# Kernel optimization log

Hardware: AMD Instinct MI355X
Metric: run time of the kernel (lower is better)

## Reference

```python
import jax, jax.numpy as jnp
import numpy as np

# ---- module config (init_kwargs) ----
B, N = 4, 1
IH, IW = 256, 704          # image_size
FH, FW = 32, 88            # feature_size
C = 80                     # out_channels
XB = (-54.0, 54.0, 0.3)
YB = (-54.0, 54.0, 0.3)
ZB = (-10.0, 10.0, 20.0)
DB = (1.0, 60.0, 0.5)
D = int((DB[1] - DB[0]) / DB[2])   # 118 depth bins
NX = (int((XB[1]-XB[0])/XB[2]), int((YB[1]-YB[0])/YB[2]), int((ZB[1]-ZB[0])/ZB[2]))  # (360,360,1)
DX = jnp.array([XB[2], YB[2], ZB[2]], jnp.float32)
BX = jnp.array([XB[0]+XB[2]/2, YB[0]+YB[2]/2, ZB[0]+ZB[2]/2], jnp.float32)


def _frustum():
    # [D, fH, fW, 3] of (pixel_x, pixel_y, depth)
    ds = jnp.broadcast_to(jnp.arange(DB[0], DB[1], DB[2], dtype=jnp.float32)[:, None, None], (D, FH, FW))
    xs = jnp.broadcast_to(jnp.linspace(0.0, IW - 1.0, FW, dtype=jnp.float32)[None, None, :], (D, FH, FW))
    ys = jnp.broadcast_to(jnp.linspace(0.0, IH - 1.0, FH, dtype=jnp.float32)[None, :, None], (D, FH, FW))
    return jnp.stack([xs, ys, ds], axis=-1)


def _get_geometry(rots, trans, intrins, post_rots, post_trans,
                  l2c_rots, l2c_trans, extra_rots, extra_trans):
    frustum = _frustum()                                       # [D,fH,fW,3]
    # undo image augmentation
    pts = frustum[None, None] - post_trans[:, :, None, None, None, :]          # [B,N,D,fH,fW,3]
    pts = jnp.einsum('bnij,bndhwj->bndhwi', jnp.linalg.inv(post_rots), pts)
    # (u*d, v*d, d)
    pts = jnp.concatenate([pts[..., :2] * pts[..., 2:3], pts[..., 2:3]], axis=-1)
    # camera -> ego (sensor2ego) combined with inverse intrinsics
    combine = jnp.einsum('bnij,bnjk->bnik', rots, jnp.linalg.inv(intrins))
    pts = jnp.einsum('bnij,bndhwj->bndhwi', combine, pts) + trans[:, :, None, None, None, :]
    # ego -> lidar via inverse of lidar2camera (passed in as lidar2ego_* in forward)
    pts = pts - l2c_trans[:, None, None, None, None, :]
    pts = jnp.einsum('bij,bndhwj->bndhwi', jnp.linalg.inv(l2c_rots), pts)
    # lidar augmentation
    pts = jnp.einsum('bij,bndhwj->bndhwi', extra_rots, pts) + extra_trans[:, None, None, None, None, :]
    return pts  # [B,N,D,fH,fW,3]


def _bev_pool(geom, x):
    Bb = x.shape[0]
    Cc = x.shape[-1]
    Np = x.size // Cc                                          # B*N*D*fH*fW
    feats = x.reshape(Np, Cc)
    # voxel coords; torch .long() truncates toward zero, astype(int32) matches
    coords = ((geom - (BX - DX / 2.0)) / DX).reshape(Np, 3).astype(jnp.int32)
    batch_ix = jnp.repeat(jnp.arange(Bb, dtype=jnp.int32), Np // Bb)
    kept = ((coords[:, 0] >= 0) & (coords[:, 0] < NX[0]) &
            (coords[:, 1] >= 0) & (coords[:, 1] < NX[1]) &
            (coords[:, 2] >= 0) & (coords[:, 2] < NX[2]))
    # zero out dropped points instead of filtering (jit-friendly, same sum)
    feats = jnp.where(kept[:, None], feats, 0.0)
    cx = jnp.clip(coords[:, 0], 0, NX[0] - 1)
    cy = jnp.clip(coords[:, 1], 0, NX[1] - 1)
    cz = jnp.clip(coords[:, 2], 0, NX[2] - 1)
    lin = ((batch_ix * NX[2] + cz) * NX[0] + cx) * NX[1] + cy
    grid = jax.ops.segment_sum(feats, lin, num_segments=Bb * NX[2] * NX[0] * NX[1])
    grid = grid.reshape(Bb, NX[2], NX[0], NX[1], Cc)           # (B, Z, X, Y, C)
    # torch: permute(0,4,1,3,2)->(B,C,Z,Y,X), unbind Z, cat on channel => z-major (B, Z*C, Y, X)
    grid = jnp.transpose(grid, (0, 1, 4, 3, 2))                # (B, Z, C, Y, X)
    return grid.reshape(Bb, NX[2] * Cc, NX[1], NX[0])


def setup_inputs() -> dict:
    key = jax.random.key(0)
    k1, k2, k3 = jax.random.split(key, 3)
    x = jax.random.normal(k1, (B, N, D, FH, FW, C), dtype=jnp.float32)
    # sensor2ego: identity (forward's fallback branch)
    rots = jnp.broadcast_to(jnp.eye(3, dtype=jnp.float32), (B, N, 3, 3))
    trans = jnp.zeros((B, N, 3), jnp.float32)
    intr = np.array([[500.0, 0.0, 352.0], [0.0, 500.0, 128.0], [0.0, 0.0, 1.0]], np.float32)
    intrins = jnp.broadcast_to(jnp.asarray(intr), (B, N, 3, 3))
    post_rots = jnp.broadcast_to(jnp.eye(3, dtype=jnp.float32), (B, N, 3, 3))
    post_trans = jax.random.uniform(k2, (B, N, 3), jnp.float32, -4.0, 4.0) * jnp.array([1.0, 1.0, 0.0], jnp.float32)
    # lidar->camera rotation: cam_x=-lid_y, cam_y=-lid_z, cam_z=lid_x
    R_lc = np.array([[0.0, -1.0, 0.0], [0.0, 0.0, -1.0], [1.0, 0.0, 0.0]], np.float32)
    lidar2ego_rots = jnp.broadcast_to(jnp.asarray(R_lc), (B, 3, 3))
    lidar2ego_trans = jnp.zeros((B, 3), jnp.float32)
    yaw = 0.05
    Rz = np.array([[np.cos(yaw), -np.sin(yaw), 0.0], [np.sin(yaw), np.cos(yaw), 0.0], [0.0, 0.0, 1.0]], np.float32)
    extra_rots = jnp.broadcast_to(jnp.asarray(Rz), (B, 3, 3))
    extra_trans = jax.random.uniform(k3, (B, 3), jnp.float32, -0.5, 0.5)
    return dict(x=x, rots=rots, trans=trans, intrins=intrins, post_rots=post_rots,
                post_trans=post_trans, lidar2ego_rots=lidar2ego_rots,
                lidar2ego_trans=lidar2ego_trans, extra_rots=extra_rots, extra_trans=extra_trans)


def reference(x, rots, trans, intrins, post_rots, post_trans,
              lidar2ego_rots, lidar2ego_trans, extra_rots, extra_trans):
    geom = _get_geometry(rots, trans, intrins, post_rots, post_trans,
                         lidar2ego_rots, lidar2ego_trans, extra_rots, extra_trans)
    return _bev_pool(geom, x)  # (B, Z*C, ny, nx) = (4, 80, 360, 360)
```

## Files before the change

kernel.cpp:

```cpp
#include <hip/hip_runtime.h>
#include <cstdint>
#include <cstddef>

#define DEVFN __device__ __forceinline__

typedef float f32x4 __attribute__((ext_vector_type(4)));
typedef int   i32x4 __attribute__((ext_vector_type(4)));

namespace {
constexpr int kB  = 4,  kN  = 1,  kD = 118, kFH = 32, kFW = 88, kC = 80;
constexpr int kIH = 256, kIW = 704;
constexpr int kNX = 360, kNY = 360;
constexpr int kCELLS   = kNX * kNY;
constexpr int kOutPerB = kC * kCELLS;
constexpr int kBDW     = kB * kN * kD * kFW;
constexpr int kCQ      = kC / 4;
constexpr int kNITEMS  = kBDW * kCQ;
constexpr int kSLOTCAP = kBDW + 4096;
constexpr int kYX4     = kCELLS / 4;
constexpr int kEXPN    = kB * kC * kYX4;
constexpr size_t kOffNslots = 0;
constexpr size_t kOffSlotId = 1024;
constexpr size_t kOffGws    = kOffSlotId + (size_t)kB * kCELLS * 4;
constexpr size_t kOffSf     = kOffGws + (size_t)kBDW * 8;
constexpr size_t kWsNeed    = kOffSf + (size_t)kSLOTCAP * kC * 4;
constexpr int kWSPLIT = 2;
constexpr int kWTILE  = kFW / kWSPLIT;
constexpr int kITEMS  = kWTILE * kCQ;
constexpr int kNBLK   = kB * kN * kD * kWSPLIT;
}

DEVFN void inv3(const double m[9], double o[9]) {
  double a = m[0], b = m[1], c = m[2];
  double d = m[3], e = m[4], f = m[5];
  double g = m[6], h = m[7], i = m[8];
  double A = e * i - f * h;
  double B = f * g - d * i;
  double C = d * h - e * g;
  double det = a * A + b * B + c * C;
  double id = 1.0 / det;
  o[0] = A * id;              o[1] = (c * h - b * i) * id;  o[2] = (b * f - c * e) * id;
  o[3] = B * id;              o[4] = (a * i - c * g) * id;  o[5] = (c * d - a * f) * id;
  o[6] = C * id;              o[7] = (b * g - a * h) * id;  o[8] = (a * e - b * d) * id;
}

DEVFN void mm3(const double a[9], const double b[9], double o[9]) {
  #pragma unroll
  for (int i = 0; i < 3; i++)
    #pragma unroll
    for (int j = 0; j < 3; j++)
      o[i * 3 + j] = a[i * 3] * b[j] + a[i * 3 + 1] * b[3 + j] + a[i * 3 + 2] * b[6 + j];
}

DEVFN void mv3(const double a[9], const double v[3], double o[3]) {
  #pragma unroll
  for (int i = 0; i < 3; i++)
    o[i] = a[i * 3] * v[0] + a[i * 3 + 1] * v[1] + a[i * 3 + 2] * v[2];
}

DEVFN double ys_of(int h) {
  return (h == kFH - 1) ? (double)(kIH - 1)
                        : (double)h * ((double)(kIH - 1) / (double)(kFH - 1));
}

DEVFN double xs_of(int w) {
  return (w == kFW - 1) ? (double)(kIW - 1)
                        : (double)w * ((double)(kIW - 1) / (double)(kFW - 1));
}

DEVFN void fold_chain(int bn, int b,
                      const float* __restrict__ rots,
                      const float* __restrict__ trans,
                      const float* __restrict__ intrins,
                      const float* __restrict__ post_rots,
                      const float* __restrict__ post_trans,
                      const float* __restrict__ l2c_rots,
                      const float* __restrict__ l2c_trans,
                      const float* __restrict__ extra_rots,
                      const float* __restrict__ extra_trans,
                      double* __restrict__ M) {
  double pr[9], it[9], rt[9], lr[9], er[9];
  #pragma unroll
  for (int k = 0; k < 9; k++) {
    pr[k] = (double)post_rots[bn * 9 + k];
    it[k] = (double)intrins[bn * 9 + k];
    rt[k] = (double)rots[bn * 9 + k];
    lr[k] = (double)l2c_rots[b * 9 + k];
    er[k] = (double)extra_rots[b * 9 + k];
  }
  double Minv[9], Ai[9], Li[9], C1[9], C2[9], A[9];
  inv3(pr, Minv); inv3(it, Ai); inv3(lr, Li);
  mm3(rt, Ai, C1); mm3(Li, C1, C2); mm3(er, C2, A);
  double tv[3], t2[3], t3[3];
  #pragma unroll
  for (int k = 0; k < 3; k++)
    tv[k] = (double)trans[bn * 3 + k] - (double)l2c_trans[b * 3 + k];
  mv3(Li, tv, t2); mv3(er, t2, t3);
  #pragma unroll
  for (int k = 0; k < 9; k++) { M[k] = Minv[k]; M[12 + k] = A[k]; }
  #pragma unroll
  for (int k = 0; k < 3; k++) {
    M[9 + k]  = (double)post_trans[bn * 3 + k];
    M[21 + k] = t3[k] + (double)extra_trans[b * 3 + k];
  }
}

DEVFN int cell_id(const double* __restrict__ M, int b,
                  double xs, double ys, double dsv) {
  const double f0 = xs - M[9], f1 = ys - M[10], f2 = dsv - M[11];
  const double v0 = M[0] * f0 + M[1] * f1 + M[2] * f2;
  const double v1 = M[3] * f0 + M[4] * f1 + M[5] * f2;
  const double v2 = M[6] * f0 + M[7] * f1 + M[8] * f2;
  const double q0 = v0 * v2, q1 = v1 * v2, q2 = v2;
  const double g0 = M[12] * q0 + M[13] * q1 + M[14] * q2 + M[21];
  const double g1 = M[15] * q0 + M[16] * q1 + M[17] * q2 + M[22];
  const double g2 = M[18] * q0 + M[19] * q1 + M[20] * q2 + M[23];
  const double lo01 = (-54.0 + 0.3 / 2.0) - 0.3 / 2.0;
  const double lo2  = (-10.0 + 20.0 / 2.0) - 20.0 / 2.0;
  const int cx = (int)((g0 - lo01) / 0.3);
  const int cy = (int)((g1 - lo01) / 0.3);
  const int cz = (int)((g2 - lo2) / 20.0);
  if (cx >= 0 && cx < kNX && cy >= 0 && cy < kNY && cz == 0)
    return b * kCELLS + cy * kNX + cx;
  return -1;
}

DEVFN int get_slot(int* __restrict__ slotid, int cell, int* __restrict__ nslots) {
  int s = ((volatile int*)slotid)[cell];
  if (s < 0) {
    const int my = atomicAdd(nslots, 1);
    if (my < kSLOTCAP) {
      const int old = atomicCAS(&slotid[cell], -1, my);
      s = (old == -1) ? my : old;
    } else {
      s = ((volatile int*)slotid)[cell];
    }
  }
  return s;
}

__global__ __launch_bounds__(256)
void init_kernel(int* __restrict__ slotid, float* __restrict__ sf,
                 int* __restrict__ nslots)
{
  const int i0 = blockIdx.x * 256 + threadIdx.x;
  const int stride = gridDim.x * 256;
  if (i0 == 0) *nslots = 0;
  i32x4* s4 = (i32x4*)slotid;
  const int nS4 = kB * kCELLS / 4;
  for (int i = i0; i < nS4; i += stride) s4[i] = i32x4{-1, -1, -1, -1};
  f32x4* f4 = (f32x4*)sf;
  const int nF4 = kSLOTCAP * kC / 4;
  const f32x4 z = {0.f, 0.f, 0.f, 0.f};
  for (int i = i0; i < nF4; i += stride) f4[i] = z;
}

__global__ __launch_bounds__(256)
void geom_kernel(const float* __restrict__ x,
                 const float* __restrict__ rots,
                 const float* __restrict__ trans,
                 const float* __restrict__ intrins,
                 const float* __restrict__ post_rots,
                 const float* __restrict__ post_trans,
                 const float* __restrict__ l2c_rots,
                 const float* __restrict__ l2c_trans,
                 const float* __restrict__ extra_rots,
                 const float* __restrict__ extra_trans,
                 int* __restrict__ slotid,
                 int2* __restrict__ gws,
                 float* __restrict__ sf,
                 int* __restrict__ nslots)
{
  __shared__ double sm[24];
  const int bn = blockIdx.y, b = bn / kN;
  if (threadIdx.x == 0)
    fold_chain(bn, b, rots, trans, intrins, post_rots, post_trans,
               l2c_rots, l2c_trans, extra_rots, extra_trans, sm);
  __syncthreads();

  const int dw = blockIdx.x * 256 + threadIdx.x;
  if (dw >= kD * kFW) return;
  const int d = dw / kFW, w = dw % kFW;
  const double xs  = xs_of(w);
  const double dsv = 1.0 + 0.5 * (double)d;

  int cell_ref = -1;
  unsigned mask = 0, extra = 0;
  for (int h = 0; h < kFH; h++) {
    const int cell = cell_id(sm, b, xs, ys_of(h), dsv);
    if (cell >= 0) {
      if (cell_ref < 0) cell_ref = cell;
      if (cell == cell_ref) mask |= 1u << h; else extra |= 1u << h;
    }
  }
  int slot = -1;
  if (cell_ref >= 0) slot = get_slot(slotid, cell_ref, nslots);
  gws[bn * kD * kFW + dw] = make_int2(slot, (int)mask);

  while (extra) {
    const int h = __ffs(extra) - 1;
    extra &= extra - 1;
    const int cell2 = cell_id(sm, b, xs, ys_of(h), dsv);
    const int s2 = get_slot(slotid, cell2, nslots);
    if (s2 >= 0) {
      const float* px = x + ((((size_t)(bn * kD + d) * kFH + h) * kFW) + w) * kC;
      for (int c = 0; c < kC; c++)
        atomicAdd(sf + (size_t)s2 * kC + c, px[c]);
    }
  }
}

__global__ __launch_bounds__(256)
void pool_kernel(const f32x4* __restrict__ x4,
                 const int2* __restrict__ gws,
                 float* __restrict__ sf)
{
  const int item = blockIdx.x * 256 + threadIdx.x;
  const int bdw = item / kCQ;
  const int cq  = item % kCQ;
  const int2 g  = gws[bdw];
  if (g.x < 0) return;
  const unsigned mask = (unsigned)g.y;

  const int bd = bdw / kFW, w = bdw % kFW;
  const f32x4* __restrict__ p =
      x4 + (size_t)bd * kFH * (kFW * kCQ) + w * kCQ + cq;

  f32x4 acc = {0.f, 0.f, 0.f, 0.f};
  #pragma unroll
  for (int h = 0; h < kFH; h++) {
    const float s = (float)((mask >> h) & 1u);
    const f32x4 v = __builtin_nontemporal_load(p + (size_t)h * (kFW * kCQ));
    acc.x = fmaf(v.x, s, acc.x);
    acc.y = fmaf(v.y, s, acc.y);
    acc.z = fmaf(v.z, s, acc.z);
    acc.w = fmaf(v.w, s, acc.w);
  }

  float* o = sf + (size_t)g.x * kC + 4 * cq;
  atomicAdd(o + 0, acc.x);
  atomicAdd(o + 1, acc.y);
  atomicAdd(o + 2, acc.z);
  atomicAdd(o + 3, acc.w);
}

__global__ __launch_bounds__(256)
void expand_kernel(const i32x4* __restrict__ slotid4,
                   const float* __restrict__ sf,
                   f32x4* __restrict__ out4)
{
  const int t = blockIdx.x * 256 + threadIdx.x;
  const int yx4 = t % kYX4;
  const int rest = t / kYX4;
  const int c = rest % kC;
  const int b = rest / kC;

  const i32x4 s = slotid4[b * kYX4 + yx4];
  f32x4 v = {0.f, 0.f, 0.f, 0.f};
  if (s.x >= 0) v.x = sf[(size_t)s.x * kC + c];
  if (s.y >= 0) v.y = sf[(size_t)s.y * kC + c];
  if (s.z >= 0) v.z = sf[(size_t)s.z * kC + c];
  if (s.w >= 0) v.w = sf[(size_t)s.w * kC + c];

  __builtin_nontemporal_store(v, &out4[(size_t)t]);
}

__global__ __launch_bounds__(256)
void zero_kernel(f32x4* __restrict__ o4, int n4)
{
  const int stride = gridDim.x * 256;
  const f32x4 z = {0.f, 0.f, 0.f, 0.f};
  for (int i = blockIdx.x * 256 + threadIdx.x; i < n4; i += stride)
    o4[i] = z;
}

__global__ __launch_bounds__(256)
void bev_pool_kernel(const float* __restrict__ x,
                     const float* __restrict__ rots,
                     const float* __restrict__ trans,
                     const float* __restrict__ intrins,
                     const float* __restrict__ post_rots,
                     const float* __restrict__ post_trans,
                     const float* __restrict__ l2c_rots,
                     const float* __restrict__ l2c_trans,
                     const float* __restrict__ extra_rots,
                     const float* __restrict__ extra_trans,
                     float* __restrict__ out)
{
  __shared__ double sm[24];
  __shared__ int      soff[kWTILE];
  __shared__ unsigned smask[kWTILE];
  __shared__ int      s_any;

  const int bid = blockIdx.x;
  const int wt  = bid & (kWSPLIT - 1);
  const int d   = (bid / kWSPLIT) % kD;
  const int bn  = bid / (kWSPLIT * kD);
  const int b   = bn / kN;
  const int tid = threadIdx.x;

  if (tid == 0) {
    s_any = 0;
    fold_chain(bn, b, rots, trans, intrins, post_rots, post_trans,
               l2c_rots, l2c_trans, extra_rots, extra_trans, sm);
  }
  __syncthreads();

  if (tid < kWTILE) {
    const int w = wt * kWTILE + tid;
    const double xs  = xs_of(w);
    const double dsv = 1.0 + 0.5 * (double)d;
    int cell_ref = -1;
    unsigned mask = 0, extra = 0;
    for (int h = 0; h < kFH; h++) {
      const int cell = cell_id(sm, b, xs, ys_of(h), dsv);
      if (cell >= 0) {
        if (cell_ref < 0) cell_ref = cell;
        if (cell == cell_ref) mask |= 1u << h; else extra |= 1u << h;
      }
    }
    soff[tid]  = (cell_ref >= 0)
               ? (cell_ref / kCELLS) * kOutPerB + (cell_ref % kCELLS) : -1;
    smask[tid] = mask;
    if (cell_ref >= 0) s_any = 1;
    while (extra) {
      const int h = __ffs(extra) - 1;
      extra &= extra - 1;
      const int cell2 = cell_id(sm, b, xs, ys_of(h), dsv);
      const int off2 = (cell2 / kCELLS) * kOutPerB + (cell2 % kCELLS);
      const float* px = x + ((((size_t)(bn * kD + d) * kFH + h) * kFW) + w) * kC;
      for (int c = 0; c < kC; c++)
        atomicAdd(out + off2 + (size_t)c * kCELLS, px[c]);
    }
  }
  __syncthreads();
  if (!s_any) return;

  const float4* __restrict__ x4 = reinterpret_cast<const float4*>(x);
  float4 acc[4];
  int      itw[4];
  unsigned msk[4];
  bool     vld[4];
  #pragma unroll
  for (int k = 0; k < 4; k++) {
    const int item = tid + 256 * k;
    vld[k] = item < kITEMS;
    itw[k] = vld[k] ? item / kCQ : 0;
    msk[k] = vld[k] ? smask[itw[k]] : 0u;
    acc[k] = make_float4(0.f, 0.f, 0.f, 0.f);
  }
  for (int h = 0; h < kFH; h++) {
    const size_t base =
        (((size_t)(bn * kD + d) * kFH + h) * kFW + wt * kWTILE) * kCQ;
    #pragma unroll
    for (int k = 0; k < 4; k++) {
      const int item = tid + 256 * k;
      if (vld[k]) {
        const float s = (float)((msk[k] >> h) & 1u);
        const float4 v = x4[base + item];
        acc[k].x = fmaf(v.x, s, acc[k].x);
        acc[k].y = fmaf(v.y, s, acc[k].y);
        acc[k].z = fmaf(v.z, s, acc[k].z);
        acc[k].w = fmaf(v.w, s, acc[k].w);
      }
    }
  }
  #pragma unroll
  for (int k = 0; k < 4; k++) {
    if (!vld[k]) continue;
    const int off = soff[itw[k]];
    if (off < 0) continue;
    const int item = tid + 256 * k;
    const int cq = item % kCQ;
    float* o = out + off + (size_t)(4 * cq) * kCELLS;
    atomicAdd(o,              acc[k].x);
    atomicAdd(o +     kCELLS, acc[k].y);
    atomicAdd(o + 2 * kCELLS, acc[k].z);
    atomicAdd(o + 3 * kCELLS, acc[k].w);
  }
}

extern "C" void kernel_launch(void* const* d_in, const int* in_sizes, int n_in,
                              void* d_out, int out_size, void* d_ws, size_t ws_size,
                              hipStream_t stream) {
  const float* x          = (const float*)d_in[0];
  const float* rots       = (const float*)d_in[1];
  const float* trans      = (const float*)d_in[2];
  const float* intrins    = (const float*)d_in[3];
  const float* post_rots  = (const float*)d_in[4];
  const float* post_trans = (const float*)d_in[5];
  const float* l2c_rots   = (const float*)d_in[6];
  const float* l2c_trans  = (const float*)d_in[7];
  const float* extra_rots = (const float*)d_in[8];
  const float* extra_trans= (const float*)d_in[9];
  float* out = (float*)d_out;

  if (ws_size >= kWsNeed) {
    char* wsb = (char*)d_ws;
    int*  nslots = (int*) (wsb + kOffNslots);
    int*  slotid = (int*) (wsb + kOffSlotId);
    int2* gws    = (int2*)(wsb + kOffGws);
    float* sf    = (float*)(wsb + kOffSf);

    init_kernel<<<dim3(1024), dim3(256), 0, stream>>>(slotid, sf, nslots);
    geom_kernel<<<dim3((kD * kFW + 255) / 256, kB * kN), dim3(256), 0, stream>>>(
        x, rots, trans, intrins, post_rots, post_trans,
        l2c_rots, l2c_trans, extra_rots, extra_trans, slotid, gws, sf, nslots);
    pool_kernel<<<dim3(kNITEMS / 256), dim3(256), 0, stream>>>(
        (const f32x4*)x, gws, sf);
    expand_kernel<<<dim3(kEXPN / 256), dim3(256), 0, stream>>>(
        (const i32x4*)slotid, sf, (f32x4*)out);
  } else {
    const int n4 = out_size / 4;
    zero_kernel<<<dim3(2048), dim3(256), 0, stream>>>((f32x4*)out, n4);
    bev_pool_kernel<<<dim3(kNBLK), dim3(256), 0, stream>>>(
        x, rots, trans, intrins, post_rots, post_trans,
        l2c_rots, l2c_trans, extra_rots, extra_trans, out);
  }
}
```

Before: 139.7 us.

## Fuse init, geometry, pooling and expansion into one cooperative kernel

Replaces the four separate launches (init, geom, pool, expand) with a single cooperative kernel of 512 blocks that separates the phases with grid-wide syncs. The goal is to remove launch overhead and inter-kernel gaps. In exchange, the heavy phases run on a fixed grid with grid-stride loops instead of one thread per item, grid.sync adds its own cost, and a device-attribute query runs on the host every call. The old multi-kernel path stays as a fallback when cooperative launch is unavailable or fails.

```diff
diff --git a/kernel.cpp b/kernel.cpp
--- a/kernel.cpp
+++ b/kernel.cpp
@@ -1,6 +1,9 @@
 #include <hip/hip_runtime.h>
+#include <hip/hip_cooperative_groups.h>
 #include <cstdint>
 #include <cstddef>
+
+namespace cg = cooperative_groups;
 
 #define DEVFN __device__ __forceinline__
 
@@ -18,8 +21,10 @@
 constexpr int kNITEMS  = kBDW * kCQ;
 constexpr int kSLOTCAP = kBDW + 4096;
 constexpr int kYX4     = kCELLS / 4;
-constexpr int kEXPN    = kB * kC * kYX4;
+constexpr int kOUT4    = kB * kC * kYX4;
+constexpr int kCoopGrid = 512;
 constexpr size_t kOffNslots = 0;
+constexpr size_t kOffGM     = 128;
 constexpr size_t kOffSlotId = 1024;
 constexpr size_t kOffGws    = kOffSlotId + (size_t)kB * kCELLS * 4;
 constexpr size_t kOffSf     = kOffGws + (size_t)kBDW * 8;
@@ -139,6 +144,131 @@
   return s;
 }
 
+__global__ __launch_bounds__(256, 2)
+void fused_kernel(const float* __restrict__ x,
+                  const float* __restrict__ rots,
+                  const float* __restrict__ trans,
+                  const float* __restrict__ intrins,
+                  const float* __restrict__ post_rots,
+                  const float* __restrict__ post_trans,
+                  const float* __restrict__ l2c_rots,
+                  const float* __restrict__ l2c_trans,
+                  const float* __restrict__ extra_rots,
+                  const float* __restrict__ extra_trans,
+                  int* __restrict__ slotid,
+                  int2* __restrict__ gws,
+                  float* __restrict__ sf,
+                  int* __restrict__ nslots,
+                  double* __restrict__ gm,
+                  f32x4* __restrict__ out4)
+{
+  cg::grid_group grid = cg::this_grid();
+  const int tid0 = blockIdx.x * 256 + threadIdx.x;
+  const int NT   = gridDim.x * 256;
+
+  if (tid0 == 0) *nslots = 0;
+  if (tid0 < kB * kN)
+    fold_chain(tid0, tid0 / kN, rots, trans, intrins, post_rots, post_trans,
+               l2c_rots, l2c_trans, extra_rots, extra_trans, gm + tid0 * 24);
+  {
+    i32x4* s4 = (i32x4*)slotid;
+    for (int i = tid0; i < kB * kCELLS / 4; i += NT)
+      s4[i] = i32x4{-1, -1, -1, -1};
+    f32x4* f4 = (f32x4*)sf;
+    const f32x4 z = {0.f, 0.f, 0.f, 0.f};
+    for (int i = tid0; i < kSLOTCAP * kC / 4; i += NT) f4[i] = z;
+  }
+  grid.sync();
+
+  for (int p = tid0; p < kBDW; p += NT) {
+    const int bn = p / (kD * kFW);
+    const int dw = p % (kD * kFW);
+    const int b  = bn / kN;
+    const int d  = dw / kFW, w = dw % kFW;
+    const double* M = gm + bn * 24;
+    const double xs  = xs_of(w);
+    const double dsv = 1.0 + 0.5 * (double)d;
+
+    int cell_ref = -1;
+    unsigned mask = 0, extra = 0;
+    for (int h = 0; h < kFH; h++) {
+      const int cell = cell_id(M, b, xs, ys_of(h), dsv);
+      if (cell >= 0) {
+        if (cell_ref < 0) cell_ref = cell;
+        if (cell == cell_ref) mask |= 1u << h; else extra |= 1u << h;
+      }
+    }
+    int slot = -1;
+    if (cell_ref >= 0) slot = get_slot(slotid, cell_ref, nslots);
+    gws[p] = make_int2(slot, (int)mask);
+
+    while (extra) {
+      const int h = __ffs(extra) - 1;
+      extra &= extra - 1;
+      const int cell2 = cell_id(M, b, xs, ys_of(h), dsv);
+      const int s2 = get_slot(slotid, cell2, nslots);
+      if (s2 >= 0) {
+        const float* px = x + ((((size_t)(bn * kD + d) * kFH + h) * kFW) + w) * kC;
+        for (int c = 0; c < kC; c++)
+          atomicAdd(sf + (size_t)s2 * kC + c, px[c]);
+      }
+    }
+  }
+  grid.sync();
+
+  {
+    const f32x4* __restrict__ x4 = (const f32x4*)x;
+    for (int item = tid0; item < kNITEMS; item += NT) {
+      const int bdw = item / kCQ;
+      const int cq  = item % kCQ;
+      const int2 g  = gws[bdw];
+      if (g.x < 0) continue;
+      const unsigned mask = (unsigned)g.y;
+
+      const int bd = bdw / kFW, w = bdw % kFW;
+      const f32x4* __restrict__ p =
+          x4 + (size_t)bd * kFH * (kFW * kCQ) + w * kCQ + cq;
+
+      f32x4 acc = {0.f, 0.f, 0.f, 0.f};
+      #pragma unroll
+      for (int h = 0; h < kFH; h++) {
+        const float s = (float)((mask >> h) & 1u);
+        const f32x4 v = __builtin_nontemporal_load(p + (size_t)h * (kFW * kCQ));
+        acc.x = fmaf(v.x, s, acc.x);
+        acc.y = fmaf(v.y, s, acc.y);
+        acc.z = fmaf(v.z, s, acc.z);
+        acc.w = fmaf(v.w, s, acc.w);
+      }
+
+      float* o = sf + (size_t)g.x * kC + 4 * cq;
+      atomicAdd(o + 0, acc.x);
+      atomicAdd(o + 1, acc.y);
+      atomicAdd(o + 2, acc.z);
+      atomicAdd(o + 3, acc.w);
+    }
+  }
+  grid.sync();
+
+  {
+    const i32x4* __restrict__ slotid4 = (const i32x4*)slotid;
+    for (int t = tid0; t < kOUT4; t += NT) {
+      const int yx4  = t % kYX4;
+      const int rest = t / kYX4;
+      const int c = rest % kC;
+      const int b = rest / kC;
+
+      const i32x4 s = slotid4[b * kYX4 + yx4];
+      f32x4 v = {0.f, 0.f, 0.f, 0.f};
+      if (s.x >= 0) v.x = sf[(size_t)s.x * kC + c];
+      if (s.y >= 0) v.y = sf[(size_t)s.y * kC + c];
+      if (s.z >= 0) v.z = sf[(size_t)s.z * kC + c];
+      if (s.w >= 0) v.w = sf[(size_t)s.w * kC + c];
+
+      __builtin_nontemporal_store(v, &out4[(size_t)t]);
+    }
+  }
+}
+
 __global__ __launch_bounds__(256)
 void init_kernel(int* __restrict__ slotid, float* __restrict__ sf,
                  int* __restrict__ nslots)
@@ -397,10 +527,34 @@
 
   if (ws_size >= kWsNeed) {
     char* wsb = (char*)d_ws;
-    int*  nslots = (int*) (wsb + kOffNslots);
-    int*  slotid = (int*) (wsb + kOffSlotId);
-    int2* gws    = (int2*)(wsb + kOffGws);
-    float* sf    = (float*)(wsb + kOffSf);
+    int*    nslots = (int*)   (wsb + kOffNslots);
+    double* gm     = (double*)(wsb + kOffGM);
+    int*    slotid = (int*)   (wsb + kOffSlotId);
+    int2*   gws    = (int2*)  (wsb + kOffGws);
+    float*  sf     = (float*) (wsb + kOffSf);
+    f32x4*  out4   = (f32x4*)out;
+
+    bool coop = false;
+    int dev = 0;
+    if (hipGetDevice(&dev) == hipSuccess) {
+      int attr = 0;
+      if (hipDeviceGetAttribute(&attr, hipDeviceAttributeCooperativeLaunch,
+                                dev) == hipSuccess && attr != 0)
+        coop = true;
+    }
+    if (coop) {
+      void* args[] = {
+        (void*)&x, (void*)&rots, (void*)&trans, (void*)&intrins,
+        (void*)&post_rots, (void*)&post_trans, (void*)&l2c_rots,
+        (void*)&l2c_trans, (void*)&extra_rots, (void*)&extra_trans,
+        (void*)&slotid, (void*)&gws, (void*)&sf, (void*)&nslots,
+        (void*)&gm, (void*)&out4};
+      hipError_t e = hipLaunchCooperativeKernel(
+          (const void*)fused_kernel, dim3(kCoopGrid), dim3(256),
+          args, 0, stream);
+      if (e == hipSuccess) return;
+      (void)hipGetLastError();
+    }
 
     init_kernel<<<dim3(1024), dim3(256), 0, stream>>>(slotid, sf, nslots);
     geom_kernel<<<dim3((kD * kFW + 255) / 256, kB * kN), dim3(256), 0, stream>>>(
@@ -408,8 +562,8 @@
         l2c_rots, l2c_trans, extra_rots, extra_trans, slotid, gws, sf, nslots);
     pool_kernel<<<dim3(kNITEMS / 256), dim3(256), 0, stream>>>(
         (const f32x4*)x, gws, sf);
-    expand_kernel<<<dim3(kEXPN / 256), dim3(256), 0, stream>>>(
-        (const i32x4*)slotid, sf, (f32x4*)out);
+    expand_kernel<<<dim3(kOUT4 / 256), dim3(256), 0, stream>>>(
+        (const i32x4*)slotid, sf, out4);
   } else {
     const int n4 = out_size / 4;
     zero_kernel<<<dim3(2048), dim3(256), 0, stream>>>((f32x4*)out, n4);
```

After: 333.4 us. 139% more time.

## Replace pool atomics with per-column partials and linked-list combine pass

Applied to the files above, without the earlier changes.

Geometry now builds a per-slot linked list of the (b,d,w) columns that map to each slot. The pool kernel writes its partial sums to a dense buffer instead of issuing float atomics. A new combine kernel walks each slot's list and adds the partials into the slot features. This removes atomic contention, at the cost of an extra kernel launch, a larger workspace, and serial pointer-chasing reads.

```diff
diff --git a/kernel.cpp b/kernel.cpp
--- a/kernel.cpp
+++ b/kernel.cpp
@@ -18,12 +18,15 @@
 constexpr int kNITEMS  = kBDW * kCQ;
 constexpr int kSLOTCAP = kBDW + 4096;
 constexpr int kYX4     = kCELLS / 4;
-constexpr int kEXPN    = kB * kC * kYX4;
+constexpr int kOUT4    = kB * kC * kYX4;
 constexpr size_t kOffNslots = 0;
 constexpr size_t kOffSlotId = 1024;
 constexpr size_t kOffGws    = kOffSlotId + (size_t)kB * kCELLS * 4;
-constexpr size_t kOffSf     = kOffGws + (size_t)kBDW * 8;
-constexpr size_t kWsNeed    = kOffSf + (size_t)kSLOTCAP * kC * 4;
+constexpr size_t kOffHead   = kOffGws  + (size_t)kBDW * 8;
+constexpr size_t kOffNext   = kOffHead + (size_t)kSLOTCAP * 4;
+constexpr size_t kOffSf     = kOffNext + (size_t)kBDW * 4;
+constexpr size_t kOffSfPb   = kOffSf   + (size_t)kSLOTCAP * kC * 4;
+constexpr size_t kWsNeed    = kOffSfPb + (size_t)kBDW * kC * 4;
 constexpr int kWSPLIT = 2;
 constexpr int kWTILE  = kFW / kWSPLIT;
 constexpr int kITEMS  = kWTILE * kCQ;
@@ -140,8 +143,8 @@
 }
 
 __global__ __launch_bounds__(256)
-void init_kernel(int* __restrict__ slotid, float* __restrict__ sf,
-                 int* __restrict__ nslots)
+void init_kernel(int* __restrict__ slotid, int* __restrict__ head,
+                 float* __restrict__ sf, int* __restrict__ nslots)
 {
   const int i0 = blockIdx.x * 256 + threadIdx.x;
   const int stride = gridDim.x * 256;
@@ -149,6 +152,9 @@
   i32x4* s4 = (i32x4*)slotid;
   const int nS4 = kB * kCELLS / 4;
   for (int i = i0; i < nS4; i += stride) s4[i] = i32x4{-1, -1, -1, -1};
+  i32x4* h4 = (i32x4*)head;
+  const int nH4 = kSLOTCAP / 4;
+  for (int i = i0; i < nH4; i += stride) h4[i] = i32x4{-1, -1, -1, -1};
   f32x4* f4 = (f32x4*)sf;
   const int nF4 = kSLOTCAP * kC / 4;
   const f32x4 z = {0.f, 0.f, 0.f, 0.f};
@@ -168,6 +174,8 @@
                  const float* __restrict__ extra_trans,
                  int* __restrict__ slotid,
                  int2* __restrict__ gws,
+                 int* __restrict__ head,
+                 int* __restrict__ next,
                  float* __restrict__ sf,
                  int* __restrict__ nslots)
 {
@@ -193,9 +201,13 @@
       if (cell == cell_ref) mask |= 1u << h; else extra |= 1u << h;
     }
   }
+  const int p = bn * kD * kFW + dw;
   int slot = -1;
-  if (cell_ref >= 0) slot = get_slot(slotid, cell_ref, nslots);
-  gws[bn * kD * kFW + dw] = make_int2(slot, (int)mask);
+  if (cell_ref >= 0) {
+    slot = get_slot(slotid, cell_ref, nslots);
+    next[p] = atomicExch(&head[slot], p);
+  }
+  gws[p] = make_int2(slot, (int)mask);
 
   while (extra) {
     const int h = __ffs(extra) - 1;
@@ -213,7 +225,7 @@
 __global__ __launch_bounds__(256)
 void pool_kernel(const f32x4* __restrict__ x4,
                  const int2* __restrict__ gws,
-                 float* __restrict__ sf)
+                 f32x4* __restrict__ sfpb4)
 {
   const int item = blockIdx.x * 256 + threadIdx.x;
   const int bdw = item / kCQ;
@@ -237,11 +249,30 @@
     acc.w = fmaf(v.w, s, acc.w);
   }
 
-  float* o = sf + (size_t)g.x * kC + 4 * cq;
-  atomicAdd(o + 0, acc.x);
-  atomicAdd(o + 1, acc.y);
-  atomicAdd(o + 2, acc.z);
-  atomicAdd(o + 3, acc.w);
+  sfpb4[item] = acc;
+}
+
+__global__ __launch_bounds__(256)
+void combine_kernel(const int* __restrict__ head,
+                    const int* __restrict__ next,
+                    const f32x4* __restrict__ sfpb4,
+                    f32x4* __restrict__ sf4)
+{
+  const int t = blockIdx.x * 256 + threadIdx.x;
+  const int slot = t / kCQ;
+  const int cq   = t % kCQ;
+  int p = head[slot];
+  if (p < 0) return;
+  f32x4 acc = {0.f, 0.f, 0.f, 0.f};
+  while (p >= 0) {
+    const f32x4 v = sfpb4[p * kCQ + cq];
+    acc.x += v.x; acc.y += v.y; acc.z += v.z; acc.w += v.w;
+    p = next[p];
+  }
+  f32x4* o = sf4 + (size_t)slot * kCQ + cq;
+  const f32x4 prev = *o;
+  acc.x += prev.x; acc.y += prev.y; acc.z += prev.z; acc.w += prev.w;
+  *o = acc;
 }
 
 __global__ __launch_bounds__(256)
@@ -397,18 +428,24 @@
 
   if (ws_size >= kWsNeed) {
     char* wsb = (char*)d_ws;
-    int*  nslots = (int*) (wsb + kOffNslots);
-    int*  slotid = (int*) (wsb + kOffSlotId);
-    int2* gws    = (int2*)(wsb + kOffGws);
-    float* sf    = (float*)(wsb + kOffSf);
-
-    init_kernel<<<dim3(1024), dim3(256), 0, stream>>>(slotid, sf, nslots);
+    int*   nslots = (int*)  (wsb + kOffNslots);
+    int*   slotid = (int*)  (wsb + kOffSlotId);
+    int2*  gws    = (int2*) (wsb + kOffGws);
+    int*   head   = (int*)  (wsb + kOffHead);
+    int*   next   = (int*)  (wsb + kOffNext);
+    float* sf     = (float*)(wsb + kOffSf);
+    f32x4* sfpb4  = (f32x4*)(wsb + kOffSfPb);
+
+    init_kernel<<<dim3(1024), dim3(256), 0, stream>>>(slotid, head, sf, nslots);
     geom_kernel<<<dim3((kD * kFW + 255) / 256, kB * kN), dim3(256), 0, stream>>>(
         x, rots, trans, intrins, post_rots, post_trans,
-        l2c_rots, l2c_trans, extra_rots, extra_trans, slotid, gws, sf, nslots);
+        l2c_rots, l2c_trans, extra_rots, extra_trans,
+        slotid, gws, head, next, sf, nslots);
     pool_kernel<<<dim3(kNITEMS / 256), dim3(256), 0, stream>>>(
-        (const f32x4*)x, gws, sf);
-    expand_kernel<<<dim3(kEXPN / 256), dim3(256), 0, stream>>>(
+        (const f32x4*)x, gws, sfpb4);
+    combine_kernel<<<dim3(kSLOTCAP * kCQ / 256), dim3(256), 0, stream>>>(
+        head, next, sfpb4, (f32x4*)sf);
+    expand_kernel<<<dim3(kOUT4 / 256), dim3(256), 0, stream>>>(
         (const i32x4*)slotid, sf, (f32x4*)out);
   } else {
     const int n4 = out_size / 4;
```

Measured after the change: 141.0 us. Within noise of the previous version (+0.9%).
